# Kernel optimization log

Hardware: AMD Instinct MI355X
Metric: run time of the kernel (lower is better)

Reference implementation:

```python
import jax, jax.numpy as jnp
import numpy as np

B, N, H = 32, 2048, 128
L4H = 4 * H  # concatenated (c0,h0,c1,h1) embedding dim


def _lstm_cell(x, c, h, Wx, Wh, b):
    g = x @ Wx + h @ Wh + b                      # [B,N,4H]
    i, f, gg, o = jnp.split(g, 4, axis=-1)
    c_new = jax.nn.sigmoid(f) * c + jax.nn.sigmoid(i) * jnp.tanh(gg)
    h_new = jax.nn.sigmoid(o) * jnp.tanh(c_new)
    return c_new, h_new


def setup_inputs() -> dict:
    key = jax.random.key(0)
    ks = jax.random.split(key, 20)
    s = 0.05
    inp = {
        'node_embeddings': jax.random.normal(ks[0], (B, N, H), jnp.float32),
        'c0': jax.random.normal(ks[1], (B, N, H), jnp.float32),
        'h0': jax.random.normal(ks[2], (B, N, H), jnp.float32),
        'c1': jax.random.normal(ks[3], (B, N, H), jnp.float32),
        'h1': jax.random.normal(ks[4], (B, N, H), jnp.float32),
        'instruction_pointer': jax.random.uniform(ks[5], (B, N), jnp.float32),
        'Wx0': s * jax.random.normal(ks[6], (H, 4 * H), jnp.float32),
        'Wh0': s * jax.random.normal(ks[7], (H, 4 * H), jnp.float32),
        'b0': jnp.zeros((4 * H,), jnp.float32),
        'Wx1': s * jax.random.normal(ks[8], (H, 4 * H), jnp.float32),
        'Wh1': s * jax.random.normal(ks[9], (H, 4 * H), jnp.float32),
        'b1': jnp.zeros((4 * H,), jnp.float32),
        'raise_W': s * jax.random.normal(ks[10], (L4H, 2), jnp.float32),
        'raise_b': jnp.zeros((2,), jnp.float32),
        'branch_W': s * jax.random.normal(ks[11], (L4H, 2), jnp.float32),
        'branch_b': jnp.zeros((2,), jnp.float32),
        'true_indexes': jax.random.randint(ks[12], (B, N), 0, N, jnp.int32),
        'false_indexes': jax.random.randint(ks[13], (B, N), 0, N, jnp.int32),
        'raise_indexes': jax.random.randint(ks[14], (B, N), 0, N, jnp.int32),
        'exit_node_indexes': jax.random.randint(ks[15], (B,), 0, N, jnp.int32),
        'raise_node_indexes': jax.random.randint(ks[16], (B,), 0, N, jnp.int32),
        'current_step': jnp.zeros((B,), jnp.int32),
        'step_limits': jax.random.randint(ks[17], (B,), 1, 100, jnp.int32),
    }
    return inp


def reference(node_embeddings, c0, h0, c1, h1, instruction_pointer,
              Wx0, Wh0, b0, Wx1, Wh1, b1, raise_W, raise_b, branch_W, branch_b,
              true_indexes, false_indexes, raise_indexes,
              exit_node_indexes, raise_node_indexes, current_step, step_limits):
    num_nodes = node_embeddings.shape[1]

    # --- execute: stacked 2-layer LSTM per node (vectorized over B,N) ---
    c0n, h0n = _lstm_cell(node_embeddings, c0, h0, Wx0, Wh0, b0)
    c1n, h1n = _lstm_cell(h0n, c1, h1, Wx1, Wh1, b1)
    old = (c0, h0, c1, h1)
    contrib = (c0n, h0n, c1n, h1n)

    # --- mask exit and raise nodes: keep old hidden state there ---
    node_ids = jnp.arange(num_nodes)[None, :]                  # [1,N]
    m_exit = node_ids == exit_node_indexes[:, None]            # [B,N]
    m_raise = node_ids == raise_node_indexes[:, None]          # [B,N]
    m_keep = (m_exit | m_raise)[..., None]                     # raise_in_ipagnn=True
    contrib = tuple(jnp.where(m_keep, o, c) for o, c in zip(old, contrib))

    # --- raise / branch decisions ---
    emb = jnp.concatenate(contrib, axis=-1)                    # [B,N,4H]
    raise_dec = jax.nn.softmax(emb @ raise_W + raise_b, axis=-1)
    raise_dec = jnp.where(m_exit[..., None], jnp.array([0.0, 1.0], raise_dec.dtype), raise_dec)
    branch_dec = jax.nn.softmax(emb @ branch_W + branch_b, axis=-1)

    p_raise = raise_dec[..., 0]
    p_noraise = raise_dec[..., 1]
    p_true = p_noraise * branch_dec[..., 0]
    p_false = p_noraise * branch_dec[..., 1]

    seg = jax.vmap(lambda d, i: jax.ops.segment_sum(d, i, num_segments=num_nodes))

    # --- instruction pointer update (scatter-add over soft edges) ---
    ip = instruction_pointer
    ip_new = (seg(p_raise * ip, raise_indexes)
              + seg(p_true * ip, true_indexes)
              + seg(p_false * ip, false_indexes))               # [B,N]

    # --- hidden-state aggregation, weighted by instruction pointer ---
    denom = (ip_new + 1e-7)[..., None]                          # [B,N,1]
    wr = (p_raise * ip)[..., None]
    wt = (p_true * ip)[..., None]
    wf = (p_false * ip)[..., None]
    agg = tuple((seg(hc * wr, raise_indexes)
                 + seg(hc * wt, true_indexes)
                 + seg(hc * wf, false_indexes)) / denom
                for hc in contrib)

    # --- keep old state if example already hit its step limit ---
    live = (current_step < step_limits)                         # [B]
    ip_fin = jnp.where(live[:, None], ip_new, ip)
    hid_fin = tuple(jnp.where(live[:, None, None], a, o) for a, o in zip(agg, old))

    # pack carry: (c0,h0,c1,h1) embedding + instruction pointer -> [B,N,4H+1]
    return jnp.concatenate(list(hid_fin) + [ip_fin[..., None]], axis=-1)
```

## Files before the change

### kernel.cpp

```cpp
#include <hip/hip_runtime.h>
#include <hip/hip_bf16.h>

constexpr int Bc  = 32;
constexpr int Nc  = 2048;
constexpr int Hc  = 128;
constexpr int H4c = 512;
constexpr int BNc = Bc * Nc;

typedef __attribute__((ext_vector_type(8))) short short8;
typedef __attribute__((ext_vector_type(4))) float f32x4;

__device__ __forceinline__ float sigf(float x)  { return 1.f / (1.f + __expf(-x)); }
__device__ __forceinline__ float tanh_(float x) { return 1.f - 2.f / (__expf(2.f * x) + 1.f); }

__device__ __forceinline__ unsigned short bfu(float f) {
    union { float f; unsigned u; } a; a.f = f;
    unsigned u = a.u;
    return (unsigned short)((u + 0x7FFFu + ((u >> 16) & 1u)) >> 16);
}
__device__ __forceinline__ float bf2f(unsigned short u) {
    union { unsigned u; float f; } a; a.u = ((unsigned)u) << 16;
    return a.f;
}
__device__ __forceinline__ unsigned cvtpk(float lo, float hi) {
    unsigned r;
    asm("v_cvt_pk_bf16_f32 %0, %1, %2" : "=v"(r) : "v"(lo), "v"(hi));
    return r;
}

__device__ __forceinline__ int a_off(int buf, int row, int byte) {
    return buf * 5120 + row * 80 + byte;
}
__device__ __forceinline__ int cs_off(int row, int unit) {
    return row * 512 + ((unit ^ (row & 7)) << 4);
}

__global__ __launch_bounds__(256) void prep_kernel(
    const float* __restrict__ Wx0, const float* __restrict__ Wh0,
    const float* __restrict__ Wx1, const float* __restrict__ Wh1,
    unsigned short* __restrict__ W0F, unsigned short* __restrict__ W1F)
{
    int idx = blockIdx.x * 256 + threadIdx.x;
    int ct = idx >> 9, ks = (idx >> 6) & 7, lane = idx & 63;
    int col = ct * 16 + (lane & 15);
    unsigned short* p0 = W0F + (size_t)idx * 8;
    unsigned short* p1 = W1F + (size_t)idx * 8;
    #pragma unroll
    for (int e = 0; e < 8; ++e) {
        int k = ks * 32 + (lane >> 4) * 8 + e;
        float v0 = (k < 128) ? Wx0[k * 512 + col] : Wh0[(k - 128) * 512 + col];
        float v1 = (k < 128) ? Wx1[k * 512 + col] : Wh1[(k - 128) * 512 + col];
        p0[e] = bfu(v0);
        p1[e] = bfu(v1);
    }
}

__global__ __launch_bounds__(512, 4) void gemm0_kernel(
    const float* __restrict__ x_in,  const float* __restrict__ c0_in,
    const float* __restrict__ h0_in, const float* __restrict__ h1_in,
    const unsigned short* __restrict__ W0F, const float* __restrict__ b0,
    const int* __restrict__ exit_i, const int* __restrict__ raise_i,
    unsigned short* __restrict__ contrib, unsigned short* __restrict__ A1F)
{
    __shared__ __align__(16) char Ab[10240];
    __shared__ __align__(16) char Cs[32768];

    const int t    = threadIdx.x;
    const int w    = t >> 6, l = t & 63, lr = l & 15, lg = l >> 4;
    const int row0 = blockIdx.x * 64;
    const int bidx = row0 >> 11;
    const int eb   = exit_i[bidx];
    const int rbn  = raise_i[bidx];
    const int j    = w * 16 + lr;

    const int srow = t >> 3, sfq = t & 7;
#define STAGE0(c, bi)                                                          \
    {                                                                          \
        const float* sp = ((c) < 4 ? x_in : h0_in)                             \
            + (size_t)(row0 + srow) * Hc + ((c) & 3) * 32 + sfq * 4;           \
        float4 v = *(const float4*)sp;                                         \
        uint2 b2 = { cvtpk(v.x, v.y), cvtpk(v.z, v.w) };                       \
        *(uint2*)(Ab + a_off(bi, srow, sfq * 8)) = b2;                         \
    }

    f32x4 acc[4][4];
    #pragma unroll
    for (int g = 0; g < 4; ++g) {
        float bv = b0[g * 128 + j];
        f32x4 vv = {bv, bv, bv, bv};
        #pragma unroll
        for (int mt = 0; mt < 4; ++mt) acc[mt][g] = vv;
    }

    STAGE0(0, 0);
    short8 bn[4];
    #pragma unroll
    for (int g = 0; g < 4; ++g)
        bn[g] = *(const short8*)(W0F + ((size_t)((g * 8 + w) * 8) * 64 + l) * 8);
    #pragma unroll
    for (int c = 0; c < 8; ++c) {
        __syncthreads();
        short8 bc[4];
        #pragma unroll
        for (int g = 0; g < 4; ++g) bc[g] = bn[g];
        if (c < 7) {
            STAGE0(c + 1, (c + 1) & 1);
            #pragma unroll
            for (int g = 0; g < 4; ++g)
                bn[g] = *(const short8*)(W0F + ((size_t)((g * 8 + w) * 8 + c + 1) * 64 + l) * 8);
        }
        short8 a[4];
        #pragma unroll
        for (int mt = 0; mt < 4; ++mt)
            a[mt] = *(const short8*)(Ab + a_off(c & 1, mt * 16 + lr, lg * 16));
        #pragma unroll
        for (int mt = 0; mt < 4; ++mt)
            #pragma unroll
            for (int g = 0; g < 4; ++g)
                acc[mt][g] = __builtin_amdgcn_mfma_f32_16x16x32_bf16(
                    a[mt], bc[g], acc[mt][g], 0, 0, 0);
    }

    unsigned hnp[4][4];
    #pragma unroll
    for (int mt = 0; mt < 4; ++mt) {
        #pragma unroll
        for (int rr = 0; rr < 4; ++rr) {
            const int row  = mt * 16 + lg * 4 + rr;
            const int grow = row0 + row;
            const int n    = grow & (Nc - 1);
            float cold = c0_in[(size_t)grow * Hc + j];
            float h1f  = h1_in[(size_t)grow * Hc + j];
            float ig = sigf(acc[mt][0][rr]);
            float fg = sigf(acc[mt][1][rr]);
            float gv = tanh_(acc[mt][2][rr]);
            float og = sigf(acc[mt][3][rr]);
            float cn = fg * cold + ig * gv;
            float hn = og * tanh_(cn);
            const bool keep = (n == eb) || (n == rbn);
            float cw = keep ? cold : cn;
            float hw = hn;
            if (keep) hw = h0_in[(size_t)grow * Hc + j];
            float cwn = __shfl_xor(cw, 1);
            float hwn = __shfl_xor(hw, 1);
            if (!(lr & 1)) {
                *(unsigned*)(Cs + cs_off(row, j >> 3) + (j & 7) * 2)        = cvtpk(cw, cwn);
                *(unsigned*)(Cs + cs_off(row, 16 + (j >> 3)) + (j & 7) * 2) = cvtpk(hw, hwn);
            }
            hnp[mt][rr] = cvtpk(hn, h1f);
        }
    }
    __syncthreads();
    #pragma unroll
    for (int i = 0; i < 4; ++i) {
        const int idx = i * 512 + t;
        const int r = idx >> 5, u = idx & 31;
        short8 v = *(const short8*)(Cs + cs_off(r, u));
        *(short8*)(contrib + (size_t)(row0 + r) * H4c + u * 8) = v;
    }
    __syncthreads();
    #pragma unroll
    for (int mt = 0; mt < 4; ++mt)
        #pragma unroll
        for (int rr = 0; rr < 4; ++rr) {
            const int row = mt * 16 + lg * 4 + rr;
            unsigned pn = __shfl_xor(hnp[mt][rr], 1);
            if (!(lr & 1)) {
                unsigned h0d = (hnp[mt][rr] & 0xFFFFu) | (pn << 16);
                unsigned h1d = (hnp[mt][rr] >> 16) | (pn & 0xFFFF0000u);
                *(unsigned*)(Cs + cs_off(row, j >> 3) + (j & 7) * 2)        = h0d;
                *(unsigned*)(Cs + cs_off(row, 16 + (j >> 3)) + (j & 7) * 2) = h1d;
            }
        }
    __syncthreads();
    #pragma unroll
    for (int i = 0; i < 4; ++i) {
        const int idx  = i * 512 + t;
        const int frag = idx >> 6;
        const int lane = idx & 63;
        const int mt = frag >> 3, ks = frag & 7;
        const int row  = mt * 16 + (lane & 15);
        const int unit = ks * 4 + (lane >> 4);
        short8 v = *(const short8*)(Cs + cs_off(row, unit));
        *(short8*)(A1F + (((size_t)blockIdx.x * 32 + frag) << 9) + (size_t)lane * 8) = v;
    }
#undef STAGE0
}

__global__ __launch_bounds__(512, 4) void gemm1_kernel(
    const unsigned short* __restrict__ A1F, const float* __restrict__ c1_in,
    const float* __restrict__ h1_in,
    const unsigned short* __restrict__ W1F, const float* __restrict__ b1,
    const float* __restrict__ rW, const float* __restrict__ rbv,
    const float* __restrict__ bW, const float* __restrict__ bbv,
    const float* __restrict__ ip_in,
    const int* __restrict__ exit_i, const int* __restrict__ raise_i,
    unsigned short* __restrict__ contrib, float* __restrict__ w_all)
{
    __shared__ __align__(16) char AsCs[32768];
    __shared__ __align__(16) float dw[2048];

    const int t    = threadIdx.x;
    const int w    = t >> 6, l = t & 63, lr = l & 15, lg = l >> 4;
    const int row0 = blockIdx.x * 64;
    const int bidx = row0 >> 11;
    const int eb   = exit_i[bidx];
    const int rbn  = raise_i[bidx];
    const int j    = w * 16 + lr;

    const unsigned short* Af = A1F + ((size_t)blockIdx.x * 32 << 9);
    #pragma unroll
    for (int c = 0; c < 4; ++c) {
        const int frag = w * 4 + c;
        __builtin_amdgcn_global_load_lds(
            (const unsigned int*)(Af + ((size_t)frag * 64 + l) * 8),
            (unsigned int*)(AsCs + frag * 1024), 16, 0, 0);
    }
    if (t < 256) {
        ((float4*)dw)[t]       = ((const float4*)rW)[t];
        ((float4*)dw)[256 + t] = ((const float4*)bW)[t];
    }

    f32x4 acc[4][4];
    #pragma unroll
    for (int g = 0; g < 4; ++g) {
        float bv = b1[g * 128 + j];
        f32x4 vv = {bv, bv, bv, bv};
        #pragma unroll
        for (int mt = 0; mt < 4; ++mt) acc[mt][g] = vv;
    }

    short8 bn[4];
    #pragma unroll
    for (int g = 0; g < 4; ++g)
        bn[g] = *(const short8*)(W1F + ((size_t)((g * 8 + w) * 8) * 64 + l) * 8);

    __syncthreads();

    #pragma unroll
    for (int ks = 0; ks < 8; ++ks) {
        short8 bc[4];
        #pragma unroll
        for (int g = 0; g < 4; ++g) bc[g] = bn[g];
        if (ks < 7) {
            #pragma unroll
            for (int g = 0; g < 4; ++g)
                bn[g] = *(const short8*)(W1F + ((size_t)((g * 8 + w) * 8 + ks + 1) * 64 + l) * 8);
        }
        short8 a[4];
        #pragma unroll
        for (int mt = 0; mt < 4; ++mt)
            a[mt] = *(const short8*)(AsCs + (mt * 8 + ks) * 1024 + l * 16);
        #pragma unroll
        for (int mt = 0; mt < 4; ++mt)
            #pragma unroll
            for (int g = 0; g < 4; ++g)
                acc[mt][g] = __builtin_amdgcn_mfma_f32_16x16x32_bf16(
                    a[mt], bc[g], acc[mt][g], 0, 0, 0);
    }
    __syncthreads();

    char* Cs = AsCs;

    #pragma unroll
    for (int mt = 0; mt < 4; ++mt) {
        #pragma unroll
        for (int rr = 0; rr < 4; ++rr) {
            const int row  = mt * 16 + lg * 4 + rr;
            const int grow = row0 + row;
            const int n    = grow & (Nc - 1);
            float cold = c1_in[(size_t)grow * Hc + j];
            float ig = sigf(acc[mt][0][rr]);
            float fg = sigf(acc[mt][1][rr]);
            float gv = tanh_(acc[mt][2][rr]);
            float og = sigf(acc[mt][3][rr]);
            float cn = fg * cold + ig * gv;
            float hn = og * tanh_(cn);
            const bool keep = (n == eb) || (n == rbn);
            float cw = keep ? cold : cn;
            float hw = hn;
            if (keep) hw = h1_in[(size_t)grow * Hc + j];
            float cwn = __shfl_xor(cw, 1);
            float hwn = __shfl_xor(hw, 1);
            if (!(lr & 1)) {
                *(unsigned*)(Cs + cs_off(row, j >> 3) + (j & 7) * 2)        = cvtpk(cw, cwn);
                *(unsigned*)(Cs + cs_off(row, 16 + (j >> 3)) + (j & 7) * 2) = cvtpk(hw, hwn);
            }
        }
    }
    __syncthreads();

    #pragma unroll
    for (int i = 0; i < 4; ++i) {
        const int idx = i * 512 + t;
        const int r = idx >> 5, u = idx & 31;
        short8 v = *(const short8*)(Cs + cs_off(r, u));
        *(short8*)(contrib + (size_t)(row0 + r) * H4c + 256 + u * 8) = v;
    }

    {
        const int r8 = l >> 3, s = l & 7;
        const int row  = w * 8 + r8;
        const int grow = row0 + row;
        float pr0 = 0.f, pr1 = 0.f, pb0 = 0.f, pb1 = 0.f;
        #pragma unroll
        for (int cu = 0; cu < 8; ++cu) {
            short8 ev;
            if (s < 4)
                ev = *(const short8*)(contrib + (size_t)grow * H4c + s * 64 + cu * 8);
            else
                ev = *(const short8*)(Cs + cs_off(row, (s - 4) * 8 + cu));
            const int col0 = s * 64 + cu * 8;
            const float4* rp = (const float4*)(dw + col0 * 2);
            const float4* bp = (const float4*)(dw + 1024 + col0 * 2);
            #pragma unroll
            for (int q = 0; q < 4; ++q) {
                float4 rv = rp[q], bv = bp[q];
                float e0 = bf2f((unsigned short)ev[q * 2]);
                float e1 = bf2f((unsigned short)ev[q * 2 + 1]);
                pr0 += e0 * rv.x + e1 * rv.z;
                pr1 += e0 * rv.y + e1 * rv.w;
                pb0 += e0 * bv.x + e1 * bv.z;
                pb1 += e0 * bv.y + e1 * bv.w;
            }
        }
        #pragma unroll
        for (int m = 1; m < 8; m <<= 1) {
            pr0 += __shfl_xor(pr0, m);
            pr1 += __shfl_xor(pr1, m);
            pb0 += __shfl_xor(pb0, m);
            pb1 += __shfl_xor(pb1, m);
        }
        if (s == 0) {
            const int n = grow & (Nc - 1);
            float r0v = pr0 + rbv[0], r1v = pr1 + rbv[1];
            float m  = fmaxf(r0v, r1v);
            float z0 = __expf(r0v - m), z1 = __expf(r1v - m);
            float inv = 1.f / (z0 + z1);
            float praise = z0 * inv, pno = z1 * inv;
            if (n == eb) { praise = 0.f; pno = 1.f; }
            float q0 = pb0 + bbv[0], q1 = pb1 + bbv[1];
            float mm = fmaxf(q0, q1);
            float y0 = __expf(q0 - mm), y1 = __expf(q1 - mm);
            float binv = 1.f / (y0 + y1);
            float ipv = ip_in[grow];
            w_all[grow]            = praise * ipv;
            w_all[BNc + grow]      = pno * y0 * binv * ipv;
            w_all[2 * BNc + grow]  = pno * y1 * binv * ipv;
        }
    }
}

__global__ __launch_bounds__(256) void build_kernel(
    const int* __restrict__ t_idx, const int* __restrict__ f_idx,
    const int* __restrict__ r_idx, int* __restrict__ head, int* __restrict__ nxt)
{
    const int row  = blockIdx.x * 256 + threadIdx.x;
    const int base = (row >> 11) << 11;
    const int e0 = row * 4;
    int o;
    o = atomicExch(&head[base + r_idx[row]], e0);     nxt[e0]     = o;
    o = atomicExch(&head[base + t_idx[row]], e0 + 1); nxt[e0 + 1] = o;
    o = atomicExch(&head[base + f_idx[row]], e0 + 2); nxt[e0 + 2] = o;
}

__global__ __launch_bounds__(256) void gather_kernel(
    const unsigned short* __restrict__ contrib, const float* __restrict__ w_all,
    const int* __restrict__ head, const int* __restrict__ nxt,
    const float* __restrict__ c0_in, const float* __restrict__ h0_in,
    const float* __restrict__ c1_in, const float* __restrict__ h1_in,
    const float* __restrict__ ip_in,
    const int* __restrict__ cstep, const int* __restrict__ slim,
    float* __restrict__ out)
{
    const int gtid = blockIdx.x * 256 + threadIdx.x;
    const int wid  = gtid >> 6;
    const int l    = gtid & 63;
    const int bidx = wid >> 11;

    float acc[8] = {0.f, 0.f, 0.f, 0.f, 0.f, 0.f, 0.f, 0.f};
    float ipsum = 0.f;

    int e = head[wid];
    while (e >= 0) {
        const int src = e >> 2;
        const float w = w_all[(e & 3) * BNc + src];
        const unsigned short* crow = contrib + (size_t)src * 512;
        #pragma unroll
        for (int q = 0; q < 8; ++q) acc[q] += w * bf2f(crow[q * 64 + l]);
        ipsum += w;
        e = nxt[e];
    }

    const bool live = cstep[bidx] < slim[bidx];
    float* orow = out + (size_t)wid * 513;
    if (live) {
        const float inv = 1.f / (ipsum + 1e-7f);
        #pragma unroll
        for (int q = 0; q < 8; ++q) orow[q * 64 + l] = acc[q] * inv;
        if (l == 0) orow[512] = ipsum;
    } else {
        #pragma unroll
        for (int q = 0; q < 8; ++q) {
            const int off = (q & 1) * 64 + l;
            const float* p = (q >> 1) == 0 ? c0_in : (q >> 1) == 1 ? h0_in
                           : (q >> 1) == 2 ? c1_in : h1_in;
            orow[q * 64 + l] = p[(size_t)wid * Hc + off];
        }
        if (l == 0) orow[512] = ip_in[wid];
    }
}

extern "C" void kernel_launch(void* const* d_in, const int* in_sizes, int n_in,
                              void* d_out, int out_size, void* d_ws, size_t ws_size,
                              hipStream_t stream) {
    const float* x     = (const float*)d_in[0];
    const float* c0    = (const float*)d_in[1];
    const float* h0    = (const float*)d_in[2];
    const float* c1    = (const float*)d_in[3];
    const float* h1    = (const float*)d_in[4];
    const float* ip    = (const float*)d_in[5];
    const float* Wx0   = (const float*)d_in[6];
    const float* Wh0   = (const float*)d_in[7];
    const float* b0    = (const float*)d_in[8];
    const float* Wx1   = (const float*)d_in[9];
    const float* Wh1   = (const float*)d_in[10];
    const float* b1    = (const float*)d_in[11];
    const float* rW    = (const float*)d_in[12];
    const float* rb    = (const float*)d_in[13];
    const float* bW    = (const float*)d_in[14];
    const float* bb    = (const float*)d_in[15];
    const int* t_idx   = (const int*)d_in[16];
    const int* f_idx   = (const int*)d_in[17];
    const int* r_idx   = (const int*)d_in[18];
    const int* exit_i  = (const int*)d_in[19];
    const int* raise_i = (const int*)d_in[20];
    const int* cstep   = (const int*)d_in[21];
    const int* slim    = (const int*)d_in[22];
    float* out = (float*)d_out;

    unsigned short* contrib = (unsigned short*)d_ws;
    unsigned short* A1F = contrib + (size_t)BNc * 512;
    unsigned short* W0F = A1F + (size_t)BNc * 256;
    unsigned short* W1F = W0F + 512 * 256;
    float* w_all = (float*)(W1F + 512 * 256);
    int*   head  = (int*)(w_all + 3 * (size_t)BNc);
    int*   nxt   = head + BNc;

    hipMemsetAsync(head, 0xFF, BNc * sizeof(int), stream);

    prep_kernel<<<64, 256, 0, stream>>>(Wx0, Wh0, Wx1, Wh1, W0F, W1F);
    gemm0_kernel<<<BNc / 64, 512, 0, stream>>>(x, c0, h0, h1, W0F, b0,
                                               exit_i, raise_i, contrib, A1F);
    gemm1_kernel<<<BNc / 64, 512, 0, stream>>>(A1F, c1, h1, W1F, b1,
                                               rW, rb, bW, bb, ip,
                                               exit_i, raise_i, contrib, w_all);
    build_kernel<<<BNc / 256, 256, 0, stream>>>(t_idx, f_idx, r_idx, head, nxt);
    gather_kernel<<<BNc / 4, 256, 0, stream>>>(contrib, w_all, head, nxt,
                                               c0, h0, c1, h1, ip, cstep, slim, out);
}
```

Baseline: 210.3 us.

## Stage full A tile once into swizzled LDS and prefetch epilogue state loads

In gemm0 the activation tile is now loaded and converted to bf16 in a single upfront pass into a 32KB swizzled LDS buffer shared with the epilogue. This replaces the per-k-step double-buffered staging with a barrier every iteration. In both gemm kernels the c/h state values needed by the epilogue are loaded into registers right after the MFMA loop, before the barrier, so their latency overlaps. The trade-off is higher register pressure and no overlap of the A-tile load with compute.

```diff
diff --git a/kernel.cpp b/kernel.cpp
--- a/kernel.cpp
+++ b/kernel.cpp
@@ -28,9 +28,6 @@
     return r;
 }
 
-__device__ __forceinline__ int a_off(int buf, int row, int byte) {
-    return buf * 5120 + row * 80 + byte;
-}
 __device__ __forceinline__ int cs_off(int row, int unit) {
     return row * 512 + ((unit ^ (row & 7)) << 4);
 }
@@ -62,8 +59,7 @@
     const int* __restrict__ exit_i, const int* __restrict__ raise_i,
     unsigned short* __restrict__ contrib, unsigned short* __restrict__ A1F)
 {
-    __shared__ __align__(16) char Ab[10240];
-    __shared__ __align__(16) char Cs[32768];
+    __shared__ __align__(16) char AsCs[32768];
 
     const int t    = threadIdx.x;
     const int w    = t >> 6, l = t & 63, lr = l & 15, lg = l >> 4;
@@ -73,14 +69,19 @@
     const int rbn  = raise_i[bidx];
     const int j    = w * 16 + lr;
 
-    const int srow = t >> 3, sfq = t & 7;
-#define STAGE0(c, bi)                                                          \
-    {                                                                          \
-        const float* sp = ((c) < 4 ? x_in : h0_in)                             \
-            + (size_t)(row0 + srow) * Hc + ((c) & 3) * 32 + sfq * 4;           \
-        float4 v = *(const float4*)sp;                                         \
-        uint2 b2 = { cvtpk(v.x, v.y), cvtpk(v.z, v.w) };                       \
-        *(uint2*)(Ab + a_off(bi, srow, sfq * 8)) = b2;                         \
+    {
+        const int r = t >> 3, q = t & 7;
+        #pragma unroll
+        for (int i = 0; i < 4; ++i) {
+            const int u = q + i * 8;
+            const float* sp = (u < 16 ? x_in : h0_in)
+                + (size_t)(row0 + r) * Hc + (u & 15) * 8;
+            float4 v0 = ((const float4*)sp)[0];
+            float4 v1 = ((const float4*)sp)[1];
+            uint4 wv = { cvtpk(v0.x, v0.y), cvtpk(v0.z, v0.w),
+                         cvtpk(v1.x, v1.y), cvtpk(v1.z, v1.w) };
+            *(uint4*)(AsCs + cs_off(r, u)) = wv;
+        }
     }
 
     f32x4 acc[4][4];
@@ -91,28 +92,27 @@
         #pragma unroll
         for (int mt = 0; mt < 4; ++mt) acc[mt][g] = vv;
     }
-
-    STAGE0(0, 0);
     short8 bn[4];
     #pragma unroll
     for (int g = 0; g < 4; ++g)
         bn[g] = *(const short8*)(W0F + ((size_t)((g * 8 + w) * 8) * 64 + l) * 8);
-    #pragma unroll
-    for (int c = 0; c < 8; ++c) {
-        __syncthreads();
+
+    __syncthreads();
+
+    #pragma unroll
+    for (int ks = 0; ks < 8; ++ks) {
         short8 bc[4];
         #pragma unroll
         for (int g = 0; g < 4; ++g) bc[g] = bn[g];
-        if (c < 7) {
-            STAGE0(c + 1, (c + 1) & 1);
+        if (ks < 7) {
             #pragma unroll
             for (int g = 0; g < 4; ++g)
-                bn[g] = *(const short8*)(W0F + ((size_t)((g * 8 + w) * 8 + c + 1) * 64 + l) * 8);
+                bn[g] = *(const short8*)(W0F + ((size_t)((g * 8 + w) * 8 + ks + 1) * 64 + l) * 8);
         }
         short8 a[4];
         #pragma unroll
         for (int mt = 0; mt < 4; ++mt)
-            a[mt] = *(const short8*)(Ab + a_off(c & 1, mt * 16 + lr, lg * 16));
+            a[mt] = *(const short8*)(AsCs + cs_off(mt * 16 + lr, ks * 4 + lg));
         #pragma unroll
         for (int mt = 0; mt < 4; ++mt)
             #pragma unroll
@@ -121,16 +121,27 @@
                     a[mt], bc[g], acc[mt][g], 0, 0, 0);
     }
 
+    float c0v[16], h1v[16];
+    #pragma unroll
+    for (int e = 0; e < 16; ++e) {
+        const int grow = row0 + (e >> 2) * 16 + lg * 4 + (e & 3);
+        c0v[e] = c0_in[(size_t)grow * Hc + j];
+        h1v[e] = h1_in[(size_t)grow * Hc + j];
+    }
+
+    __syncthreads();
+    char* Cs = AsCs;
+
     unsigned hnp[4][4];
     #pragma unroll
     for (int mt = 0; mt < 4; ++mt) {
         #pragma unroll
         for (int rr = 0; rr < 4; ++rr) {
+            const int e    = mt * 4 + rr;
             const int row  = mt * 16 + lg * 4 + rr;
             const int grow = row0 + row;
             const int n    = grow & (Nc - 1);
-            float cold = c0_in[(size_t)grow * Hc + j];
-            float h1f  = h1_in[(size_t)grow * Hc + j];
+            float cold = c0v[e];
             float ig = sigf(acc[mt][0][rr]);
             float fg = sigf(acc[mt][1][rr]);
             float gv = tanh_(acc[mt][2][rr]);
@@ -147,7 +158,7 @@
                 *(unsigned*)(Cs + cs_off(row, j >> 3) + (j & 7) * 2)        = cvtpk(cw, cwn);
                 *(unsigned*)(Cs + cs_off(row, 16 + (j >> 3)) + (j & 7) * 2) = cvtpk(hw, hwn);
             }
-            hnp[mt][rr] = cvtpk(hn, h1f);
+            hnp[mt][rr] = cvtpk(hn, h1v[e]);
         }
     }
     __syncthreads();
@@ -184,7 +195,6 @@
         short8 v = *(const short8*)(Cs + cs_off(row, unit));
         *(short8*)(A1F + (((size_t)blockIdx.x * 32 + frag) << 9) + (size_t)lane * 8) = v;
     }
-#undef STAGE0
 }
 
 __global__ __launch_bounds__(512, 4) void gemm1_kernel(
@@ -229,7 +239,6 @@
         #pragma unroll
         for (int mt = 0; mt < 4; ++mt) acc[mt][g] = vv;
     }
-
     short8 bn[4];
     #pragma unroll
     for (int g = 0; g < 4; ++g)
@@ -258,18 +267,26 @@
                 acc[mt][g] = __builtin_amdgcn_mfma_f32_16x16x32_bf16(
                     a[mt], bc[g], acc[mt][g], 0, 0, 0);
     }
-    __syncthreads();
-
+
+    float c1v[16];
+    #pragma unroll
+    for (int e = 0; e < 16; ++e) {
+        const int grow = row0 + (e >> 2) * 16 + lg * 4 + (e & 3);
+        c1v[e] = c1_in[(size_t)grow * Hc + j];
+    }
+
+    __syncthreads();
     char* Cs = AsCs;
 
     #pragma unroll
     for (int mt = 0; mt < 4; ++mt) {
         #pragma unroll
         for (int rr = 0; rr < 4; ++rr) {
+            const int e    = mt * 4 + rr;
             const int row  = mt * 16 + lg * 4 + rr;
             const int grow = row0 + row;
             const int n    = grow & (Nc - 1);
-            float cold = c1_in[(size_t)grow * Hc + j];
+            float cold = c1v[e];
             float ig = sigf(acc[mt][0][rr]);
             float fg = sigf(acc[mt][1][rr]);
             float gv = tanh_(acc[mt][2][rr]);
```

After: 219.7 us. 4.4% more time.

## Halve GEMM row tile to 32 rows and stage full A tile once

Applied to the files above, without the earlier changes.

Both LSTM GEMM kernels now process 32 rows per block instead of 64, doubling the grid and halving per-block accumulators and shared memory. gemm0 also loads the whole bf16 A tile (x and h0) into swizzled shared memory up front, dropping the double-buffered per-k staging and the per-iteration barriers. The aim is higher occupancy and fewer syncs. The cost is that each block reloads the full weight matrix for half as many rows, so weight traffic per row doubles. The A1F fragment layout and the logit reduction are adjusted to match.

```diff
diff --git a/kernel.cpp b/kernel.cpp
--- a/kernel.cpp
+++ b/kernel.cpp
@@ -28,9 +28,6 @@
     return r;
 }
 
-__device__ __forceinline__ int a_off(int buf, int row, int byte) {
-    return buf * 5120 + row * 80 + byte;
-}
 __device__ __forceinline__ int cs_off(int row, int unit) {
     return row * 512 + ((unit ^ (row & 7)) << 4);
 }
@@ -62,68 +59,72 @@
     const int* __restrict__ exit_i, const int* __restrict__ raise_i,
     unsigned short* __restrict__ contrib, unsigned short* __restrict__ A1F)
 {
-    __shared__ __align__(16) char Ab[10240];
-    __shared__ __align__(16) char Cs[32768];
+    __shared__ __align__(16) char AsCs[16384];
 
     const int t    = threadIdx.x;
     const int w    = t >> 6, l = t & 63, lr = l & 15, lg = l >> 4;
-    const int row0 = blockIdx.x * 64;
+    const int row0 = blockIdx.x * 32;
     const int bidx = row0 >> 11;
     const int eb   = exit_i[bidx];
     const int rbn  = raise_i[bidx];
     const int j    = w * 16 + lr;
 
-    const int srow = t >> 3, sfq = t & 7;
-#define STAGE0(c, bi)                                                          \
-    {                                                                          \
-        const float* sp = ((c) < 4 ? x_in : h0_in)                             \
-            + (size_t)(row0 + srow) * Hc + ((c) & 3) * 32 + sfq * 4;           \
-        float4 v = *(const float4*)sp;                                         \
-        uint2 b2 = { cvtpk(v.x, v.y), cvtpk(v.z, v.w) };                       \
-        *(uint2*)(Ab + a_off(bi, srow, sfq * 8)) = b2;                         \
-    }
-
-    f32x4 acc[4][4];
+    {
+        const int r = t >> 4, q = t & 15;
+        const float4* xp = (const float4*)(x_in  + (size_t)(row0 + r) * Hc + q * 8);
+        const float4* hp = (const float4*)(h0_in + (size_t)(row0 + r) * Hc + q * 8);
+        float4 x0 = xp[0], x1 = xp[1];
+        float4 h0v = hp[0], h1v_ = hp[1];
+        uint4 xw = { cvtpk(x0.x, x0.y), cvtpk(x0.z, x0.w),
+                     cvtpk(x1.x, x1.y), cvtpk(x1.z, x1.w) };
+        uint4 hw = { cvtpk(h0v.x, h0v.y), cvtpk(h0v.z, h0v.w),
+                     cvtpk(h1v_.x, h1v_.y), cvtpk(h1v_.z, h1v_.w) };
+        *(uint4*)(AsCs + cs_off(r, q))      = xw;
+        *(uint4*)(AsCs + cs_off(r, 16 + q)) = hw;
+    }
+
+    f32x4 acc[2][4];
     #pragma unroll
     for (int g = 0; g < 4; ++g) {
         float bv = b0[g * 128 + j];
         f32x4 vv = {bv, bv, bv, bv};
-        #pragma unroll
-        for (int mt = 0; mt < 4; ++mt) acc[mt][g] = vv;
-    }
-
-    STAGE0(0, 0);
+        acc[0][g] = vv;
+        acc[1][g] = vv;
+    }
     short8 bn[4];
     #pragma unroll
     for (int g = 0; g < 4; ++g)
         bn[g] = *(const short8*)(W0F + ((size_t)((g * 8 + w) * 8) * 64 + l) * 8);
-    #pragma unroll
-    for (int c = 0; c < 8; ++c) {
-        __syncthreads();
+
+    __syncthreads();
+
+    #pragma unroll
+    for (int ks = 0; ks < 8; ++ks) {
         short8 bc[4];
         #pragma unroll
         for (int g = 0; g < 4; ++g) bc[g] = bn[g];
-        if (c < 7) {
-            STAGE0(c + 1, (c + 1) & 1);
+        if (ks < 7) {
             #pragma unroll
             for (int g = 0; g < 4; ++g)
-                bn[g] = *(const short8*)(W0F + ((size_t)((g * 8 + w) * 8 + c + 1) * 64 + l) * 8);
-        }
-        short8 a[4];
-        #pragma unroll
-        for (int mt = 0; mt < 4; ++mt)
-            a[mt] = *(const short8*)(Ab + a_off(c & 1, mt * 16 + lr, lg * 16));
-        #pragma unroll
-        for (int mt = 0; mt < 4; ++mt)
+                bn[g] = *(const short8*)(W0F + ((size_t)((g * 8 + w) * 8 + ks + 1) * 64 + l) * 8);
+        }
+        short8 a[2];
+        a[0] = *(const short8*)(AsCs + cs_off(lr,      ks * 4 + lg));
+        a[1] = *(const short8*)(AsCs + cs_off(16 + lr, ks * 4 + lg));
+        #pragma unroll
+        for (int mt = 0; mt < 2; ++mt)
             #pragma unroll
             for (int g = 0; g < 4; ++g)
                 acc[mt][g] = __builtin_amdgcn_mfma_f32_16x16x32_bf16(
                     a[mt], bc[g], acc[mt][g], 0, 0, 0);
     }
 
-    unsigned hnp[4][4];
-    #pragma unroll
-    for (int mt = 0; mt < 4; ++mt) {
+    __syncthreads();
+    char* Cs = AsCs;
+
+    unsigned hnp[2][4];
+    #pragma unroll
+    for (int mt = 0; mt < 2; ++mt) {
         #pragma unroll
         for (int rr = 0; rr < 4; ++rr) {
             const int row  = mt * 16 + lg * 4 + rr;
@@ -152,7 +153,7 @@
     }
     __syncthreads();
     #pragma unroll
-    for (int i = 0; i < 4; ++i) {
+    for (int i = 0; i < 2; ++i) {
         const int idx = i * 512 + t;
         const int r = idx >> 5, u = idx & 31;
         short8 v = *(const short8*)(Cs + cs_off(r, u));
@@ -160,7 +161,7 @@
     }
     __syncthreads();
     #pragma unroll
-    for (int mt = 0; mt < 4; ++mt)
+    for (int mt = 0; mt < 2; ++mt)
         #pragma unroll
         for (int rr = 0; rr < 4; ++rr) {
             const int row = mt * 16 + lg * 4 + rr;
@@ -174,7 +175,7 @@
         }
     __syncthreads();
     #pragma unroll
-    for (int i = 0; i < 4; ++i) {
+    for (int i = 0; i < 2; ++i) {
         const int idx  = i * 512 + t;
         const int frag = idx >> 6;
         const int lane = idx & 63;
@@ -182,9 +183,8 @@
         const int row  = mt * 16 + (lane & 15);
         const int unit = ks * 4 + (lane >> 4);
         short8 v = *(const short8*)(Cs + cs_off(row, unit));
-        *(short8*)(A1F + (((size_t)blockIdx.x * 32 + frag) << 9) + (size_t)lane * 8) = v;
-    }
-#undef STAGE0
+        *(short8*)(A1F + (((size_t)blockIdx.x * 16 + frag) << 9) + (size_t)lane * 8) = v;
+    }
 }
 
 __global__ __launch_bounds__(512, 4) void gemm1_kernel(
@@ -197,21 +197,21 @@
     const int* __restrict__ exit_i, const int* __restrict__ raise_i,
     unsigned short* __restrict__ contrib, float* __restrict__ w_all)
 {
-    __shared__ __align__(16) char AsCs[32768];
+    __shared__ __align__(16) char AsCs[16384];
     __shared__ __align__(16) float dw[2048];
 
     const int t    = threadIdx.x;
     const int w    = t >> 6, l = t & 63, lr = l & 15, lg = l >> 4;
-    const int row0 = blockIdx.x * 64;
+    const int row0 = blockIdx.x * 32;
     const int bidx = row0 >> 11;
     const int eb   = exit_i[bidx];
     const int rbn  = raise_i[bidx];
     const int j    = w * 16 + lr;
 
-    const unsigned short* Af = A1F + ((size_t)blockIdx.x * 32 << 9);
-    #pragma unroll
-    for (int c = 0; c < 4; ++c) {
-        const int frag = w * 4 + c;
+    const unsigned short* Af = A1F + ((size_t)blockIdx.x * 16 << 9);
+    #pragma unroll
+    for (int c = 0; c < 2; ++c) {
+        const int frag = w * 2 + c;
         __builtin_amdgcn_global_load_lds(
             (const unsigned int*)(Af + ((size_t)frag * 64 + l) * 8),
             (unsigned int*)(AsCs + frag * 1024), 16, 0, 0);
@@ -221,15 +221,14 @@
         ((float4*)dw)[256 + t] = ((const float4*)bW)[t];
     }
 
-    f32x4 acc[4][4];
+    f32x4 acc[2][4];
     #pragma unroll
     for (int g = 0; g < 4; ++g) {
         float bv = b1[g * 128 + j];
         f32x4 vv = {bv, bv, bv, bv};
-        #pragma unroll
-        for (int mt = 0; mt < 4; ++mt) acc[mt][g] = vv;
-    }
-
+        acc[0][g] = vv;
+        acc[1][g] = vv;
+    }
     short8 bn[4];
     #pragma unroll
     for (int g = 0; g < 4; ++g)
@@ -247,23 +246,22 @@
             for (int g = 0; g < 4; ++g)
                 bn[g] = *(const short8*)(W1F + ((size_t)((g * 8 + w) * 8 + ks + 1) * 64 + l) * 8);
         }
-        short8 a[4];
-        #pragma unroll
-        for (int mt = 0; mt < 4; ++mt)
-            a[mt] = *(const short8*)(AsCs + (mt * 8 + ks) * 1024 + l * 16);
-        #pragma unroll
-        for (int mt = 0; mt < 4; ++mt)
+        short8 a[2];
+        a[0] = *(const short8*)(AsCs + (0 * 8 + ks) * 1024 + l * 16);
+        a[1] = *(const short8*)(AsCs + (1 * 8 + ks) * 1024 + l * 16);
+        #pragma unroll
+        for (int mt = 0; mt < 2; ++mt)
             #pragma unroll
             for (int g = 0; g < 4; ++g)
                 acc[mt][g] = __builtin_amdgcn_mfma_f32_16x16x32_bf16(
                     a[mt], bc[g], acc[mt][g], 0, 0, 0);
     }
-    __syncthreads();
-
+
+    __syncthreads();
     char* Cs = AsCs;
 
     #pragma unroll
-    for (int mt = 0; mt < 4; ++mt) {
+    for (int mt = 0; mt < 2; ++mt) {
         #pragma unroll
         for (int rr = 0; rr < 4; ++rr) {
             const int row  = mt * 16 + lg * 4 + rr;
@@ -291,7 +289,7 @@
     __syncthreads();
 
     #pragma unroll
-    for (int i = 0; i < 4; ++i) {
+    for (int i = 0; i < 2; ++i) {
         const int idx = i * 512 + t;
         const int r = idx >> 5, u = idx & 31;
         short8 v = *(const short8*)(Cs + cs_off(r, u));
@@ -299,18 +297,19 @@
     }
 
     {
-        const int r8 = l >> 3, s = l & 7;
-        const int row  = w * 8 + r8;
+        const int r16 = l >> 4;
+        const int s   = l & 15;
+        const int row  = w * 4 + r16;
         const int grow = row0 + row;
         float pr0 = 0.f, pr1 = 0.f, pb0 = 0.f, pb1 = 0.f;
         #pragma unroll
-        for (int cu = 0; cu < 8; ++cu) {
+        for (int cu = 0; cu < 4; ++cu) {
             short8 ev;
-            if (s < 4)
-                ev = *(const short8*)(contrib + (size_t)grow * H4c + s * 64 + cu * 8);
+            if (s < 8)
+                ev = *(const short8*)(contrib + (size_t)grow * H4c + s * 32 + cu * 8);
             else
-                ev = *(const short8*)(Cs + cs_off(row, (s - 4) * 8 + cu));
-            const int col0 = s * 64 + cu * 8;
+                ev = *(const short8*)(Cs + cs_off(row, (s - 8) * 4 + cu));
+            const int col0 = s * 32 + cu * 8;
             const float4* rp = (const float4*)(dw + col0 * 2);
             const float4* bp = (const float4*)(dw + 1024 + col0 * 2);
             #pragma unroll
@@ -325,7 +324,7 @@
             }
         }
         #pragma unroll
-        for (int m = 1; m < 8; m <<= 1) {
+        for (int m = 1; m < 16; m <<= 1) {
             pr0 += __shfl_xor(pr0, m);
             pr1 += __shfl_xor(pr1, m);
             pb0 += __shfl_xor(pb0, m);
@@ -450,9 +449,9 @@
     hipMemsetAsync(head, 0xFF, BNc * sizeof(int), stream);
 
     prep_kernel<<<64, 256, 0, stream>>>(Wx0, Wh0, Wx1, Wh1, W0F, W1F);
-    gemm0_kernel<<<BNc / 64, 512, 0, stream>>>(x, c0, h0, h1, W0F, b0,
+    gemm0_kernel<<<BNc / 32, 512, 0, stream>>>(x, c0, h0, h1, W0F, b0,
                                                exit_i, raise_i, contrib, A1F);
-    gemm1_kernel<<<BNc / 64, 512, 0, stream>>>(A1F, c1, h1, W1F, b1,
+    gemm1_kernel<<<BNc / 32, 512, 0, stream>>>(A1F, c1, h1, W1F, b1,
                                                rW, rb, bW, bb, ip,
                                                exit_i, raise_i, contrib, w_all);
     build_kernel<<<BNc / 256, 256, 0, stream>>>(t_idx, f_idx, r_idx, head, nxt);
```

Result: slower. 248.8 us (+18.3%).
